# Performance work log

Hardware: AMD Instinct MI355X
Metric: run time of the kernel (lower is better)

Reference implementation:

```python
import jax, jax.numpy as jnp
import numpy as np

B, S, H, NH, PF, L = 2, 2048, 1024, 16, 4096, 6
HD = H // NH
EPS = 1e-5


def setup_inputs() -> dict:
    key = jax.random.key(0)
    ks = jax.random.split(key, 12)
    s = lambda k, shp, fan: jax.random.normal(k, shp, jnp.float32) * (1.0 / np.sqrt(fan))
    return {
        "input_tensor": jax.random.normal(ks[0], (B, S, H), jnp.float32),
        "pos_emb": s(ks[1], (S, H), H),
        "Wq": s(ks[2], (L, H, H), H), "bq": jnp.zeros((L, H), jnp.float32),
        "Wk": s(ks[3], (L, H, H), H), "bk": jnp.zeros((L, H), jnp.float32),
        "Wv": s(ks[4], (L, H, H), H), "bv": jnp.zeros((L, H), jnp.float32),
        "Wo": s(ks[5], (L, H, H), H), "bo": jnp.zeros((L, H), jnp.float32),
        "ln_g": jnp.ones((L, H), jnp.float32), "ln_b": jnp.zeros((L, H), jnp.float32),
        "W1": s(ks[6], (L, H, PF), H), "b1": jnp.zeros((L, PF), jnp.float32),
        "W2": s(ks[7], (L, PF, H), PF), "b2": jnp.zeros((L, H), jnp.float32),
    }


def _layernorm(x, g, b):
    mu = jnp.mean(x, axis=-1, keepdims=True)
    var = jnp.mean(jnp.square(x - mu), axis=-1, keepdims=True)
    return (x - mu) * jax.lax.rsqrt(var + EPS) * g + b


def _encoder(input_tensor, pos_emb, params):
    # pos embed: same positions for every batch row
    src = input_tensor * jnp.sqrt(jnp.float32(H)) + pos_emb[None, :, :]

    def layer(src, p):
        Wq, bq, Wk, bk, Wv, bv, Wo, bo, g, b, W1, b1, W2, b2 = p
        q = (src @ Wq + bq).reshape(B, S, NH, HD)
        k = (src @ Wk + bk).reshape(B, S, NH, HD)
        v = (src @ Wv + bv).reshape(B, S, NH, HD)
        # scores [B, NH, S, S]
        energy = jnp.einsum("bqhd,bkhd->bhqk", q, k) / jnp.sqrt(jnp.float32(HD))
        attn = jax.nn.softmax(energy, axis=-1)
        ctx = jnp.einsum("bhqk,bkhd->bqhd", attn, v).reshape(B, S, H)
        attn_out = ctx @ Wo + bo
        src = _layernorm(src + attn_out, g, b)
        ffn = jax.nn.relu(src @ W1 + b1) @ W2 + b2
        src = _layernorm(src + ffn, g, b)  # same LayerNorm reused, as in source
        return src, None

    src, _ = jax.lax.scan(layer, src, params)
    return src


def reference(input_tensor, pos_emb, Wq, bq, Wk, bk, Wv, bv, Wo, bo, ln_g, ln_b, W1, b1, W2, b2):
    params = (Wq, bq, Wk, bk, Wv, bv, Wo, bo, ln_g, ln_b, W1, b1, W2, b2)
    return _encoder(input_tensor, pos_emb, params)
```

## Files before the change

kernel.cpp:

```cpp
#include <hip/hip_runtime.h>
#include <cstdint>

constexpr int Bc = 2, Sc = 2048, Hc = 1024, NHc = 16, HDc = 64, PFc = 4096, Lc = 6;
constexpr float EPSc = 1e-5f;
constexpr float QSC = 0.18033688011112042f;

using f32x4  = __attribute__((ext_vector_type(4))) float;
using bf16x8 = __attribute__((ext_vector_type(8))) __bf16;
using bf16x4 = __attribute__((ext_vector_type(4))) __bf16;
using u32x4  = __attribute__((ext_vector_type(4))) unsigned;

#if __has_builtin(__builtin_amdgcn_exp2f)
#define EXP2(x) __builtin_amdgcn_exp2f(x)
#else
#define EXP2(x) exp2f(x)
#endif

__device__ __forceinline__ f32x4 mfma16(bf16x8 a, bf16x8 b, f32x4 c) {
    return __builtin_amdgcn_mfma_f32_16x16x32_bf16(a, b, c, 0, 0, 0);
}

__device__ __forceinline__ void gload_lds16(const void* g, void* l) {
    __builtin_amdgcn_global_load_lds(
        (__attribute__((address_space(1))) void*)(uintptr_t)g,
        (__attribute__((address_space(3))) void*)(uint32_t)(uintptr_t)l,
        16, 0, 0);
}

template<int N> __device__ __forceinline__ void wait_vmcnt() {
    if constexpr (N == 0)      asm volatile("s_waitcnt vmcnt(0)" ::: "memory");
    else if constexpr (N == 6) asm volatile("s_waitcnt vmcnt(6)" ::: "memory");
    else if constexpr (N == 8) asm volatile("s_waitcnt vmcnt(8)" ::: "memory");
}
__device__ __forceinline__ void wait_lgkm0() {
    asm volatile("s_waitcnt lgkmcnt(0)" ::: "memory");
    __builtin_amdgcn_sched_barrier(0);
}

struct HL { __bf16 h, l; };
__device__ __forceinline__ HL split2(float v) {
    HL r;
    r.h = (__bf16)v;
    r.l = (__bf16)(v - (float)r.h);
    return r;
}

__device__ __forceinline__ unsigned bfbits(__bf16 x) {
    return (unsigned)__builtin_bit_cast(unsigned short, x);
}
__device__ __forceinline__ unsigned packbf(float a, float b) {
    return bfbits((__bf16)a) | (bfbits((__bf16)b) << 16);
}

__device__ __forceinline__ int xcd_swz(int bid, int nwg) {
    return (bid & 7) * (nwg >> 3) + (bid >> 3);
}

__global__ __launch_bounds__(256) void wconv_kernel(
    const float* __restrict__ in, __bf16* __restrict__ out, int K, int N)
{
    __shared__ float tile[64][65];
    const int t = threadIdx.x;
    const size_t lstride = (size_t)K * N;
    const float* ip = in + (size_t)blockIdx.z * lstride;
    __bf16* op = out + (size_t)blockIdx.z * lstride;
    const int n0 = blockIdx.x * 64, k0 = blockIdx.y * 64;
    #pragma unroll
    for (int c = 0; c < 4; ++c) {
        int idx = c * 256 + t;
        int row = idx >> 4;
        int c4  = idx & 15;
        float4 v = *(const float4*)(ip + (size_t)(k0 + row) * N + n0 + c4 * 4);
        tile[row][c4 * 4 + 0] = v.x; tile[row][c4 * 4 + 1] = v.y;
        tile[row][c4 * 4 + 2] = v.z; tile[row][c4 * 4 + 3] = v.w;
    }
    __syncthreads();
    #pragma unroll
    for (int c = 0; c < 4; ++c) {
        int idx = c * 256 + t;
        int n  = idx >> 4;
        int k4 = idx & 15;
        bf16x4 hh = { (__bf16)tile[k4 * 4 + 0][n], (__bf16)tile[k4 * 4 + 1][n],
                      (__bf16)tile[k4 * 4 + 2][n], (__bf16)tile[k4 * 4 + 3][n] };
        *(bf16x4*)(op + (size_t)(n0 + n) * K + k0 + k4 * 4) = hh;
    }
}

__global__ __launch_bounds__(256) void wconv2_kernel(
    const float* __restrict__ in, __bf16* __restrict__ outh,
    __bf16* __restrict__ outl, int K, int N)
{
    __shared__ float tile[64][65];
    const int t = threadIdx.x;
    const int n0 = blockIdx.x * 64, k0 = blockIdx.y * 64;
    #pragma unroll
    for (int c = 0; c < 4; ++c) {
        int idx = c * 256 + t;
        int row = idx >> 4;
        int c4  = idx & 15;
        float4 v = *(const float4*)(in + (size_t)(k0 + row) * N + n0 + c4 * 4);
        tile[row][c4 * 4 + 0] = v.x; tile[row][c4 * 4 + 1] = v.y;
        tile[row][c4 * 4 + 2] = v.z; tile[row][c4 * 4 + 3] = v.w;
    }
    __syncthreads();
    #pragma unroll
    for (int c = 0; c < 4; ++c) {
        int idx = c * 256 + t;
        int n  = idx >> 4;
        int k4 = idx & 15;
        HL e0 = split2(tile[k4 * 4 + 0][n]);
        HL e1 = split2(tile[k4 * 4 + 1][n]);
        HL e2 = split2(tile[k4 * 4 + 2][n]);
        HL e3 = split2(tile[k4 * 4 + 3][n]);
        bf16x4 hh = { e0.h, e1.h, e2.h, e3.h };
        bf16x4 ll = { e0.l, e1.l, e2.l, e3.l };
        *(bf16x4*)(outh + (size_t)(n0 + n) * K + k0 + k4 * 4) = hh;
        *(bf16x4*)(outl + (size_t)(n0 + n) * K + k0 + k4 * 4) = ll;
    }
}

__global__ __launch_bounds__(256) void embed_kernel(
    const float* __restrict__ in, const float* __restrict__ pos,
    float* __restrict__ sf, __bf16* __restrict__ sh, __bf16* __restrict__ sl)
{
    const int n4 = (Bc * Sc * Hc) / 4;
    const int pmask = (Sc * Hc / 4) - 1;
    for (int i = blockIdx.x * 256 + threadIdx.x; i < n4; i += gridDim.x * 256) {
        float4 a = ((const float4*)in)[i];
        float4 p = ((const float4*)pos)[i & pmask];
        float4 r;
        r.x = a.x * 32.f + p.x; r.y = a.y * 32.f + p.y;
        r.z = a.z * 32.f + p.z; r.w = a.w * 32.f + p.w;
        ((float4*)sf)[i] = r;
        HL e0 = split2(r.x), e1 = split2(r.y), e2 = split2(r.z), e3 = split2(r.w);
        bf16x4 hh = { e0.h, e1.h, e2.h, e3.h };
        bf16x4 ll = { e0.l, e1.l, e2.l, e3.l };
        ((bf16x4*)sh)[i] = hh;
        ((bf16x4*)sl)[i] = ll;
    }
}

template<int BM, int OUTMODE, bool RELU>
__global__ __launch_bounds__(256) void gemm_bt_kernel(
    const __bf16* __restrict__ A, const __bf16* __restrict__ Wt,
    const float* __restrict__ bias, void* __restrict__ out,
    int M, int N, int K)
{
    constexpr int MI = BM / 32;
    constexpr int LPT = BM / 32 + 4;
    __shared__ alignas(16) __bf16 Alds[2][BM * 64];
    __shared__ alignas(16) __bf16 Blds[2][128 * 64];

    const int tid = threadIdx.x, lane = tid & 63, wave = tid >> 6;
    const int lr = lane & 15, lg = lane >> 4;
    const int nbx = gridDim.x;
    const int swz = xcd_swz(blockIdx.y * nbx + blockIdx.x, nbx * gridDim.y);
    const int m0 = (swz / nbx) * BM, n0 = (swz % nbx) * 128;
    const int wm = (wave >> 1) * (BM / 2), wn = (wave & 1) * 64;

    f32x4 acc[MI][4] = {};

    auto stage = [&](int k0, int buf) {
        #pragma unroll
        for (int c = 0; c < BM / 32; ++c) {
            int li = c * 256 + tid;
            int row = li >> 3;
            int lcb = ((li & 7) << 4) ^ ((row & 7) << 4);
            gload_lds16(A + (size_t)(m0 + row) * K + k0 + (lcb >> 1),
                        (char*)Alds[buf] + (size_t)(c * 256 + wave * 64) * 16);
        }
        #pragma unroll
        for (int c = 0; c < 4; ++c) {
            int li = c * 256 + tid;
            int row = li >> 3;
            int lcb = ((li & 7) << 4) ^ ((row & 7) << 4);
            gload_lds16(Wt + (size_t)(n0 + row) * K + k0 + (lcb >> 1),
                        (char*)Blds[buf] + (size_t)(c * 256 + wave * 64) * 16);
        }
    };

    stage(0, 0);
    if (K > 64) stage(64, 1);

    for (int k0 = 0; k0 < K; k0 += 64) {
        const int cur = (k0 >> 6) & 1;
        if (k0 + 64 < K) wait_vmcnt<LPT>();
        else             wait_vmcnt<0>();
        __builtin_amdgcn_s_barrier();

        bf16x8 af[2][MI], bfr[2][4];
        #pragma unroll
        for (int ks = 0; ks < 2; ++ks) {
            #pragma unroll
            for (int i = 0; i < MI; ++i) {
                int ra = wm + i * 16 + lr;
                int pa = (ks * 64 + lg * 16) ^ ((ra & 7) << 4);
                af[ks][i] = *(const bf16x8*)((const char*)Alds[cur] + ra * 128 + pa);
            }
            #pragma unroll
            for (int i = 0; i < 4; ++i) {
                int rb = wn + i * 16 + lr;
                int pb = (ks * 64 + lg * 16) ^ ((rb & 7) << 4);
                bfr[ks][i] = *(const bf16x8*)((const char*)Blds[cur] + rb * 128 + pb);
            }
        }
        wait_lgkm0();
        __builtin_amdgcn_s_barrier();
        if (k0 + 128 < K) stage(k0 + 128, cur);

        __builtin_amdgcn_s_setprio(1);
        #pragma unroll
        for (int ks = 0; ks < 2; ++ks)
            #pragma unroll
            for (int mi = 0; mi < MI; ++mi)
                #pragma unroll
                for (int ni = 0; ni < 4; ++ni)
                    acc[mi][ni] = mfma16(af[ks][mi], bfr[ks][ni], acc[mi][ni]);
        __builtin_amdgcn_s_setprio(0);
    }

    #pragma unroll
    for (int ni = 0; ni < 4; ++ni) {
        int col = n0 + wn + ni * 16 + lr;
        float bv = bias[col];
        #pragma unroll
        for (int mi = 0; mi < MI; ++mi) {
            int rowb = m0 + wm + mi * 16 + lg * 4;
            #pragma unroll
            for (int r = 0; r < 4; ++r) {
                float v = acc[mi][ni][r] + bv;
                if (RELU) v = fmaxf(v, 0.f);
                size_t idx = (size_t)(rowb + r) * N + col;
                if constexpr (OUTMODE == 0) ((float*)out)[idx] = v;
                else                        ((__bf16*)out)[idx] = (__bf16)v;
            }
        }
    }
}

template<int OUTMODE, bool RELU>
__global__ __launch_bounds__(512) void gemm_bt256_kernel(
    const __bf16* __restrict__ A, const __bf16* __restrict__ Wt,
    const float* __restrict__ bias, void* __restrict__ out,
    int M, int N, int K)
{
    constexpr int LPT = 6;
    __shared__ alignas(16) __bf16 Alds[2][256 * 64];
    __shared__ alignas(16) __bf16 Blds[2][128 * 64];

    const int tid = threadIdx.x, lane = tid & 63, wave = tid >> 6;
    const int lr = lane & 15, lg = lane >> 4;
    const int nbx = gridDim.x;
    const int swz = xcd_swz(blockIdx.y * nbx + blockIdx.x, nbx * gridDim.y);
    const int m0 = (swz / nbx) * 256, n0 = (swz % nbx) * 128;
    const int wm = (wave >> 1) * 64, wn = (wave & 1) * 64;

    f32x4 acc[4][4] = {};

    auto stage = [&](int k0, int buf) {
        #pragma unroll
        for (int c = 0; c < 4; ++c) {
            int li = c * 512 + tid;
            int row = li >> 3;
            int lcb = ((li & 7) << 4) ^ ((row & 7) << 4);
            gload_lds16(A + (size_t)(m0 + row) * K + k0 + (lcb >> 1),
                        (char*)Alds[buf] + (size_t)(c * 512 + wave * 64) * 16);
        }
        #pragma unroll
        for (int c = 0; c < 2; ++c) {
            int li = c * 512 + tid;
            int row = li >> 3;
            int lcb = ((li & 7) << 4) ^ ((row & 7) << 4);
            gload_lds16(Wt + (size_t)(n0 + row) * K + k0 + (lcb >> 1),
                        (char*)Blds[buf] + (size_t)(c * 512 + wave * 64) * 16);
        }
    };

    stage(0, 0);
    if (K > 64) stage(64, 1);

    for (int k0 = 0; k0 < K; k0 += 64) {
        const int cur = (k0 >> 6) & 1;
        if (k0 + 64 < K) wait_vmcnt<LPT>();
        else             wait_vmcnt<0>();
        __builtin_amdgcn_s_barrier();

        bf16x8 af[2][4], bfr[2][4];
        #pragma unroll
        for (int ks = 0; ks < 2; ++ks) {
            #pragma unroll
            for (int i = 0; i < 4; ++i) {
                int ra = wm + i * 16 + lr;
                int pa = (ks * 64 + lg * 16) ^ ((ra & 7) << 4);
                af[ks][i] = *(const bf16x8*)((const char*)Alds[cur] + ra * 128 + pa);
                int rb = wn + i * 16 + lr;
                int pb = (ks * 64 + lg * 16) ^ ((rb & 7) << 4);
                bfr[ks][i] = *(const bf16x8*)((const char*)Blds[cur] + rb * 128 + pb);
            }
        }
        wait_lgkm0();
        __builtin_amdgcn_s_barrier();
        if (k0 + 128 < K) stage(k0 + 128, cur);

        __builtin_amdgcn_s_setprio(1);
        #pragma unroll
        for (int ks = 0; ks < 2; ++ks)
            #pragma unroll
            for (int mi = 0; mi < 4; ++mi)
                #pragma unroll
                for (int ni = 0; ni < 4; ++ni)
                    acc[mi][ni] = mfma16(af[ks][mi], bfr[ks][ni], acc[mi][ni]);
        __builtin_amdgcn_s_setprio(0);
    }

    #pragma unroll
    for (int ni = 0; ni < 4; ++ni) {
        int col = n0 + wn + ni * 16 + lr;
        float bv = bias[col];
        #pragma unroll
        for (int mi = 0; mi < 4; ++mi) {
            int rowb = m0 + wm + mi * 16 + lg * 4;
            #pragma unroll
            for (int r = 0; r < 4; ++r) {
                float v = acc[mi][ni][r] + bv;
                if (RELU) v = fmaxf(v, 0.f);
                size_t idx = (size_t)(rowb + r) * N + col;
                if constexpr (OUTMODE == 0) ((float*)out)[idx] = v;
                else                        ((__bf16*)out)[idx] = (__bf16)v;
            }
        }
    }
}

struct QKVBT {
    const __bf16 *wq, *wk, *wv;
    const float *bq, *bk, *bv;
    __bf16 *q, *k, *v;
};

__global__ __launch_bounds__(256) void qkv_bt_kernel(
    const __bf16* __restrict__ A, QKVBT a)
{
    constexpr int N = Hc, K = Hc;
    constexpr int LPT = 8;
    __shared__ alignas(16) __bf16 Alds[2][128 * 64];
    __shared__ alignas(16) __bf16 Blds[2][128 * 64];

    const int tid = threadIdx.x, lane = tid & 63, wave = tid >> 6;
    const int lr = lane & 15, lg = lane >> 4;
    const int nbx = gridDim.x;
    const int swz = xcd_swz(blockIdx.y * nbx + blockIdx.x, nbx * gridDim.y);
    const int gx = swz % nbx;
    const int widx = gx >> 3;
    const int n0 = (gx & 7) * 128;
    const int m0 = (swz / nbx) * 128;
    const int wm = (wave >> 1) * 64, wn = (wave & 1) * 64;

    const __bf16* Wt  = (widx == 0) ? a.wq : (widx == 1) ? a.wk : a.wv;
    const float* bias = (widx == 0) ? a.bq : (widx == 1) ? a.bk : a.bv;

    f32x4 acc[4][4] = {};

    auto stage = [&](int k0, int buf) {
        #pragma unroll
        for (int c = 0; c < 4; ++c) {
            int li = c * 256 + tid;
            int row = li >> 3;
            int lcb = ((li & 7) << 4) ^ ((row & 7) << 4);
            gload_lds16(A + (size_t)(m0 + row) * K + k0 + (lcb >> 1),
                        (char*)Alds[buf] + (size_t)(c * 256 + wave * 64) * 16);
            gload_lds16(Wt + (size_t)(n0 + row) * K + k0 + (lcb >> 1),
                        (char*)Blds[buf] + (size_t)(c * 256 + wave * 64) * 16);
        }
    };

    stage(0, 0);
    stage(64, 1);

    for (int k0 = 0; k0 < K; k0 += 64) {
        const int cur = (k0 >> 6) & 1;
        if (k0 + 64 < K) wait_vmcnt<LPT>();
        else             wait_vmcnt<0>();
        __builtin_amdgcn_s_barrier();

        bf16x8 af[2][4], bfr[2][4];
        #pragma unroll
        for (int ks = 0; ks < 2; ++ks) {
            #pragma unroll
            for (int i = 0; i < 4; ++i) {
                int ra = wm + i * 16 + lr;
                int pa = (ks * 64 + lg * 16) ^ ((ra & 7) << 4);
                af[ks][i] = *(const bf16x8*)((const char*)Alds[cur] + ra * 128 + pa);
                int rb = wn + i * 16 + lr;
                int pb = (ks * 64 + lg * 16) ^ ((rb & 7) << 4);
                bfr[ks][i] = *(const bf16x8*)((const char*)Blds[cur] + rb * 128 + pb);
            }
        }
        wait_lgkm0();
        __builtin_amdgcn_s_barrier();
        if (k0 + 128 < K) stage(k0 + 128, cur);

        __builtin_amdgcn_s_setprio(1);
        #pragma unroll
        for (int ks = 0; ks < 2; ++ks)
            #pragma unroll
            for (int mi = 0; mi < 4; ++mi)
                #pragma unroll
                for (int ni = 0; ni < 4; ++ni)
                    acc[mi][ni] = mfma16(af[ks][mi], bfr[ks][ni], acc[mi][ni]);
        __builtin_amdgcn_s_setprio(0);
    }

    __bf16* outp = (widx == 0) ? a.q : (widx == 1) ? a.k : a.v;
    const float osc = (widx == 0) ? QSC : 1.f;
    #pragma unroll
    for (int ni = 0; ni < 4; ++ni) {
        int col = n0 + wn + ni * 16 + lr;
        float bv = bias[col];
        int hh = col >> 6, d = col & 63;
        #pragma unroll
        for (int mi = 0; mi < 4; ++mi) {
            int rowb = m0 + wm + mi * 16 + lg * 4;
            #pragma unroll
            for (int r = 0; r < 4; ++r) {
                int row = rowb + r;
                int bb = row >> 11, s = row & (Sc - 1);
                outp[((size_t)(bb * NHc + hh) * Sc + s) * HDc + d] =
                    (__bf16)((acc[mi][ni][r] + bv) * osc);
            }
        }
    }
}

struct QKV0S {
    const __bf16 *wqh, *wql, *wkh, *wkl, *wv;
    const float *bq, *bk, *bv;
    __bf16 *qh, *ql, *kh, *kl, *vv;
};

__global__ __launch_bounds__(256) void qkv0s_kernel(
    const __bf16* __restrict__ Ahi, const __bf16* __restrict__ Alo, QKV0S a)
{
    constexpr int N = Hc, K = Hc;
    __shared__ alignas(16) __bf16 AldsH[128 * 64];
    __shared__ alignas(16) __bf16 AldsL[128 * 64];
    __shared__ alignas(16) __bf16 BldsH[128 * 64];
    __shared__ alignas(16) __bf16 BldsL[128 * 64];

    const int tid = threadIdx.x, lane = tid & 63, wave = tid >> 6;
    const int lr = lane & 15, lg = lane >> 4;
    const int nbx = gridDim.x;
    const int swz = xcd_swz(blockIdx.y * nbx + blockIdx.x, nbx * gridDim.y);
    const int gx = swz % nbx;
    const int widx = gx >> 3;
    const int n0 = (gx & 7) * 128;
    const int m0 = (swz / nbx) * 128;
    const int wm = (wave >> 1) * 64, wn = (wave & 1) * 64;
    const bool SPLIT = (widx < 2);

    const __bf16* Bh = (widx == 0) ? a.wqh : (widx == 1) ? a.wkh : a.wv;
    const __bf16* Bl = (widx == 0) ? a.wql : a.wkl;
    const float* bias = (widx == 0) ? a.bq : (widx == 1) ? a.bk : a.bv;

    f32x4 acc[4][4] = {};

    for (int k0 = 0; k0 < K; k0 += 64) {
        #pragma unroll
        for (int c = 0; c < 4; ++c) {
            int li = c * 256 + tid;
            int row = li >> 3;
            int lcb = ((li & 7) << 4) ^ ((row & 7) << 4);
            size_t aoff = (size_t)(m0 + row) * K + k0 + (lcb >> 1);
            size_t boff = (size_t)(n0 + row) * K + k0 + (lcb >> 1);
            size_t loff = (size_t)(c * 256 + wave * 64) * 16;
            gload_lds16(Ahi + aoff, (char*)AldsH + loff);
            gload_lds16(Bh + boff, (char*)BldsH + loff);
            if (SPLIT) {
                gload_lds16(Alo + aoff, (char*)AldsL + loff);
                gload_lds16(Bl + boff, (char*)BldsL + loff);
            }
        }
        __syncthreads();

        bf16x8 ah[2][4], al[2][4], bh[2][4], bl[2][4];
        #pragma unroll
        for (int ks = 0; ks < 2; ++ks) {
            #pragma unroll
            for (int i = 0; i < 4; ++i) {
                int ra = wm + i * 16 + lr;
                int pa = (ks * 64 + lg * 16) ^ ((ra & 7) << 4);
                ah[ks][i] = *(const bf16x8*)((const char*)AldsH + ra * 128 + pa);
                int rb = wn + i * 16 + lr;
                int pb = (ks * 64 + lg * 16) ^ ((rb & 7) << 4);
                bh[ks][i] = *(const bf16x8*)((const char*)BldsH + rb * 128 + pb);
                if (SPLIT) {
                    al[ks][i] = *(const bf16x8*)((const char*)AldsL + ra * 128 + pa);
                    bl[ks][i] = *(const bf16x8*)((const char*)BldsL + rb * 128 + pb);
                }
            }
        }
        #pragma unroll
        for (int ks = 0; ks < 2; ++ks)
            #pragma unroll
            for (int mi = 0; mi < 4; ++mi)
                #pragma unroll
                for (int ni = 0; ni < 4; ++ni) {
                    acc[mi][ni] = mfma16(ah[ks][mi], bh[ks][ni], acc[mi][ni]);
                    if (SPLIT) {
                        acc[mi][ni] = mfma16(al[ks][mi], bh[ks][ni], acc[mi][ni]);
                        acc[mi][ni] = mfma16(ah[ks][mi], bl[ks][ni], acc[mi][ni]);
                    }
                }
        __syncthreads();
    }

    __bf16* outh = (widx == 0) ? a.qh : (widx == 1) ? a.kh : a.vv;
    __bf16* outl = (widx == 0) ? a.ql : a.kl;
    const float osc = (widx == 0) ? QSC : 1.f;
    #pragma unroll
    for (int ni = 0; ni < 4; ++ni) {
        int col = n0 + wn + ni * 16 + lr;
        float bv = bias[col];
        int hh = col >> 6, d = col & 63;
        #pragma unroll
        for (int mi = 0; mi < 4; ++mi) {
            int rowb = m0 + wm + mi * 16 + lg * 4;
            #pragma unroll
            for (int r = 0; r < 4; ++r) {
                int row = rowb + r;
                int bb = row >> 11, s = row & (Sc - 1);
                size_t idx = ((size_t)(bb * NHc + hh) * Sc + s) * HDc + d;
                float v = (acc[mi][ni][r] + bv) * osc;
                if (SPLIT) {
                    HL e = split2(v);
                    outh[idx] = e.h;
                    outl[idx] = e.l;
                } else {
                    outh[idx] = (__bf16)v;
                }
            }
        }
    }
}

template<int QKSPLIT, int NH2>
__global__ __launch_bounds__(256) void attn_kernel(
    const __bf16* __restrict__ Qh, const __bf16* __restrict__ Ql,
    const __bf16* __restrict__ Kh, const __bf16* __restrict__ Kl,
    const __bf16* __restrict__ V, __bf16* __restrict__ O)
{
    constexpr int KVB = 64 * NH2;
    __shared__ alignas(16) __bf16 Ksh[2][KVB * 64];
    __shared__ alignas(16) __bf16 Klo[QKSPLIT ? 2 : 1][QKSPLIT ? 64 * 64 : 8];
    __shared__ alignas(16) __bf16 VT[2][NH2][64 * 64];

    const int tid = threadIdx.x;
    const int lane = tid & 63, wave = tid >> 6;
    const int lr = lane & 15, lg = lane >> 4;
    const int flat = blockIdx.x;
    const int hb = flat & 31;
    const int h = hb & 15, b = hb >> 4;
    const int q0 = (flat >> 5) * 128 + wave * 32;

    const size_t headoff = ((size_t)b * NHc + h) * Sc * HDc;
    const __bf16* Qb  = Qh + headoff;
    const __bf16* Kb  = Kh + headoff;
    const __bf16* Klb = QKSPLIT ? (Kl + headoff) : nullptr;
    const __bf16* Vb  = V + headoff;

    const size_t qrowA = (size_t)(q0 + lr) * HDc;
    const size_t qrowB = qrowA + 16 * HDc;
    bf16x8 qfA0 = *(const bf16x8*)(Qb + qrowA + lg * 8);
    bf16x8 qfA1 = *(const bf16x8*)(Qb + qrowA + 32 + lg * 8);
    bf16x8 qfB0 = *(const bf16x8*)(Qb + qrowB + lg * 8);
    bf16x8 qfB1 = *(const bf16x8*)(Qb + qrowB + 32 + lg * 8);
    bf16x8 qlA0, qlA1, qlB0, qlB1;
    if constexpr (QKSPLIT) {
        const __bf16* Qlb = Ql + headoff;
        qlA0 = *(const bf16x8*)(Qlb + qrowA + lg * 8);
        qlA1 = *(const bf16x8*)(Qlb + qrowA + 32 + lg * 8);
        qlB0 = *(const bf16x8*)(Qlb + qrowB + lg * 8);
        qlB1 = *(const bf16x8*)(Qlb + qrowB + 32 + lg * 8);
    }

    const int kp = tid & 31, dblk = tid >> 5;
    const int sp = (kp & 0x11) | ((kp & 0x06) << 1) | ((kp & 0x08) >> 2);

    auto stageK = [&](int kt, int buf) {
        #pragma unroll
        for (int c = 0; c < 2 * NH2; ++c) {
            int li  = c * 256 + tid;
            int row = li >> 3;
            int lcb = ((li & 7) << 4) ^ ((row & 7) << 4);
            size_t goff = (size_t)(kt * KVB + row) * HDc + (lcb >> 1);
            size_t loff = (size_t)(c * 256 + wave * 64) * 16;
            gload_lds16(Kb + goff, (char*)Ksh[buf] + loff);
            if constexpr (QKSPLIT)
                gload_lds16(Klb + goff, (char*)Klo[buf] + loff);
        }
    };
    auto loadV = [&](int kt, int half, bf16x8& va, bf16x8& vb2) {
        const __bf16* vs = Vb + (size_t)(kt * KVB + half * 64 + 2 * kp) * HDc + dblk * 8;
        va  = *(const bf16x8*)vs;
        vb2 = *(const bf16x8*)(vs + HDc);
    };
    auto writeVT = [&](int buf, int half, bf16x8 va, bf16x8 vb2) {
        #pragma unroll
        for (int j = 0; j < 8; ++j) {
            int d = dblk * 8 + j;
            unsigned u = bfbits(va[j]) | (bfbits(vb2[j]) << 16);
            int byte = d * 128 + ((sp * 4) ^ ((d & 7) << 4));
            *(unsigned*)((char*)VT[buf][half] + byte) = u;
        }
    };

    f32x4 oA[4] = {}, oB[4] = {};
    float mA = -1e30f, mB = -1e30f, lsA = 0.f, lsB = 0.f;

    stageK(0, 0);
    {
        bf16x8 va, vb2;
        #pragma unroll
        for (int hf = 0; hf < NH2; ++hf) {
            loadV(0, hf, va, vb2);
            writeVT(0, hf, va, vb2);
        }
    }
    __syncthreads();

    const int NT = Sc / KVB;
    int cur = 0;
    for (int kt = 0; kt < NT; ++kt) {
        const int nb = cur ^ 1;
        const bool pf = (kt + 1 < NT);
        bf16x8 va[NH2], vb2[NH2];
        if (pf) {
            stageK(kt + 1, nb);
            #pragma unroll
            for (int hf = 0; hf < NH2; ++hf) loadV(kt + 1, hf, va[hf], vb2[hf]);
        }

        const char* Kc  = (const char*)Ksh[cur];
        const char* Klc = (const char*)Klo[QKSPLIT ? cur : 0];

        #pragma unroll
        for (int half = 0; half < NH2; ++half) {
            f32x4 sA[4], sB[4];
            __builtin_amdgcn_s_setprio(1);
            #pragma unroll
            for (int kg = 0; kg < 4; ++kg) {
                int ra = half * 64 + kg * 16 + lr;
                int pa0 = (lg * 16) ^ ((ra & 7) << 4);
                int pa1 = (64 + lg * 16) ^ ((ra & 7) << 4);
                bf16x8 kf0 = *(const bf16x8*)(Kc + ra * 128 + pa0);
                bf16x8 kf1 = *(const bf16x8*)(Kc + ra * 128 + pa1);
                f32x4 tA = {}, tB = {};
                tA = mfma16(kf0, qfA0, tA);
                tA = mfma16(kf1, qfA1, tA);
                tB = mfma16(kf0, qfB0, tB);
                tB = mfma16(kf1, qfB1, tB);
                if constexpr (QKSPLIT) {
                    bf16x8 kg0 = *(const bf16x8*)(Klc + ra * 128 + pa0);
                    bf16x8 kg1 = *(const bf16x8*)(Klc + ra * 128 + pa1);
                    tA = mfma16(kg0, qfA0, tA);
                    tA = mfma16(kg1, qfA1, tA);
                    tA = mfma16(kf0, qlA0, tA);
                    tA = mfma16(kf1, qlA1, tA);
                    tB = mfma16(kg0, qfB0, tB);
                    tB = mfma16(kg1, qfB1, tB);
                    tB = mfma16(kf0, qlB0, tB);
                    tB = mfma16(kf1, qlB1, tB);
                }
                sA[kg] = tA;
                sB[kg] = tB;
            }
            __builtin_amdgcn_s_setprio(0);

            float mtA = -1e30f, mtB = -1e30f;
            #pragma unroll
            for (int kg = 0; kg < 4; ++kg)
                #pragma unroll
                for (int r = 0; r < 4; ++r) {
                    mtA = fmaxf(mtA, sA[kg][r]);
                    mtB = fmaxf(mtB, sB[kg][r]);
                }
            mtA = fmaxf(mtA, __shfl_xor(mtA, 16));
            mtA = fmaxf(mtA, __shfl_xor(mtA, 32));
            mtB = fmaxf(mtB, __shfl_xor(mtB, 16));
            mtB = fmaxf(mtB, __shfl_xor(mtB, 32));
            if (!__all(mtA <= mA + 8.f)) {
                float mnew = fmaxf(mA, mtA);
                float fac = EXP2(mA - mnew);
                mA = mnew;
                lsA *= fac;
                #pragma unroll
                for (int r = 0; r < 4; ++r) {
                    float fr = __shfl(fac, (lg << 4) | (lg * 4 + r));
                    #pragma unroll
                    for (int nd = 0; nd < 4; ++nd) oA[nd][r] *= fr;
                }
            }
            if (!__all(mtB <= mB + 8.f)) {
                float mnew = fmaxf(mB, mtB);
                float fac = EXP2(mB - mnew);
                mB = mnew;
                lsB *= fac;
                #pragma unroll
                for (int r = 0; r < 4; ++r) {
                    float fr = __shfl(fac, (lg << 4) | (lg * 4 + r));
                    #pragma unroll
                    for (int nd = 0; nd < 4; ++nd) oB[nd][r] *= fr;
                }
            }
            float psA = 0.f, psB = 0.f;
            #pragma unroll
            for (int kg = 0; kg < 4; ++kg)
                #pragma unroll
                for (int r = 0; r < 4; ++r) {
                    float pA = EXP2(sA[kg][r] - mA);
                    float pB = EXP2(sB[kg][r] - mB);
                    psA += pA;
                    psB += pB;
                    sA[kg][r] = pA;
                    sB[kg][r] = pB;
                }
            psA += __shfl_xor(psA, 16);
            psA += __shfl_xor(psA, 32);
            psB += __shfl_xor(psB, 16);
            psB += __shfl_xor(psB, 32);
            lsA += psA;
            lsB += psB;

            #pragma unroll
            for (int kh2 = 0; kh2 < 2; ++kh2) {
                u32x4 pkA, pkB;
                pkA[0] = packbf(sA[2 * kh2][0],     sA[2 * kh2][1]);
                pkA[1] = packbf(sA[2 * kh2][2],     sA[2 * kh2][3]);
                pkA[2] = packbf(sA[2 * kh2 + 1][0], sA[2 * kh2 + 1][1]);
                pkA[3] = packbf(sA[2 * kh2 + 1][2], sA[2 * kh2 + 1][3]);
                pkB[0] = packbf(sB[2 * kh2][0],     sB[2 * kh2][1]);
                pkB[1] = packbf(sB[2 * kh2][2],     sB[2 * kh2][3]);
                pkB[2] = packbf(sB[2 * kh2 + 1][0], sB[2 * kh2 + 1][1]);
                pkB[3] = packbf(sB[2 * kh2 + 1][2], sB[2 * kh2 + 1][3]);
                bf16x8 pafA = __builtin_bit_cast(bf16x8, pkA);
                bf16x8 pafB = __builtin_bit_cast(bf16x8, pkB);
                __builtin_amdgcn_s_setprio(1);
                #pragma unroll
                for (int nd = 0; nd < 4; ++nd) {
                    int d = nd * 16 + lr;
                    int byte = d * 128 + ((64 * kh2 + 16 * lg) ^ ((d & 7) << 4));
                    bf16x8 vbf = *(const bf16x8*)((const char*)VT[cur][half] + byte);
                    oA[nd] = mfma16(pafA, vbf, oA[nd]);
                    oB[nd] = mfma16(pafB, vbf, oB[nd]);
                }
                __builtin_amdgcn_s_setprio(0);
            }
        }

        if (pf) {
            #pragma unroll
            for (int hf = 0; hf < NH2; ++hf) writeVT(nb, hf, va[hf], vb2[hf]);
        }
        __syncthreads();
        cur = nb;
    }

    #pragma unroll
    for (int r = 0; r < 4; ++r) {
        float lvA = __shfl(lsA, (lg << 4) | (lg * 4 + r));
        float lvB = __shfl(lsB, (lg << 4) | (lg * 4 + r));
        float invA = 1.f / lvA;
        float invB = 1.f / lvB;
        size_t orowA = ((size_t)b * Sc + q0 + lg * 4 + r) * Hc + h * HDc;
        size_t orowB = orowA + (size_t)16 * Hc;
        #pragma unroll
        for (int nd = 0; nd < 4; ++nd) {
            O[orowA + nd * 16 + lr] = (__bf16)(oA[nd][r] * invA);
            O[orowB + nd * 16 + lr] = (__bf16)(oB[nd][r] * invB);
        }
    }
}

__global__ __launch_bounds__(256) void ln_kernel(
    const float* __restrict__ xr, const __bf16* __restrict__ y,
    const float* __restrict__ g, const float* __restrict__ beta,
    float* __restrict__ of, __bf16* __restrict__ oh)
{
    __shared__ float red[2][4];
    const int row = blockIdx.x, t = threadIdx.x;
    const int lane = t & 63, wave = t >> 6;
    const int idx = row * 256 + t;
    float4 a = ((const float4*)xr)[idx];
    bf16x4 cb = ((const bf16x4*)y)[idx];
    float4 v;
    v.x = a.x + (float)cb[0]; v.y = a.y + (float)cb[1];
    v.z = a.z + (float)cb[2]; v.w = a.w + (float)cb[3];
    float s1 = v.x + v.y + v.z + v.w;
    float s2 = v.x * v.x + v.y * v.y + v.z * v.z + v.w * v.w;
    #pragma unroll
    for (int off = 1; off < 64; off <<= 1) {
        s1 += __shfl_xor(s1, off);
        s2 += __shfl_xor(s2, off);
    }
    if (lane == 0) { red[0][wave] = s1; red[1][wave] = s2; }
    __syncthreads();
    s1 = red[0][0] + red[0][1] + red[0][2] + red[0][3];
    s2 = red[1][0] + red[1][1] + red[1][2] + red[1][3];
    const float mu   = s1 * (1.f / Hc);
    const float var  = s2 * (1.f / Hc) - mu * mu;
    const float rstd = rsqrtf(var + EPSc);
    float4 gg = ((const float4*)g)[t];
    float4 bb = ((const float4*)beta)[t];
    float4 r;
    r.x = (v.x - mu) * rstd * gg.x + bb.x;
    r.y = (v.y - mu) * rstd * gg.y + bb.y;
    r.z = (v.z - mu) * rstd * gg.z + bb.z;
    r.w = (v.w - mu) * rstd * gg.w + bb.w;
    ((float4*)of)[idx] = r;
    bf16x4 hh = { (__bf16)r.x, (__bf16)r.y, (__bf16)r.z, (__bf16)r.w };
    ((bf16x4*)oh)[idx] = hh;
}

extern "C" void kernel_launch(void* const* d_in, const int* in_sizes, int n_in,
                              void* d_out, int out_size, void* d_ws, size_t ws_size,
                              hipStream_t stream)
{
    const float* inp = (const float*)d_in[0];
    const float* pos = (const float*)d_in[1];
    const float* Wq  = (const float*)d_in[2];
    const float* bq  = (const float*)d_in[3];
    const float* Wk  = (const float*)d_in[4];
    const float* bk  = (const float*)d_in[5];
    const float* Wv  = (const float*)d_in[6];
    const float* bv  = (const float*)d_in[7];
    const float* Wo  = (const float*)d_in[8];
    const float* bo  = (const float*)d_in[9];
    const float* lng = (const float*)d_in[10];
    const float* lnb = (const float*)d_in[11];
    const float* W1  = (const float*)d_in[12];
    const float* b1  = (const float*)d_in[13];
    const float* W2  = (const float*)d_in[14];
    const float* b2  = (const float*)d_in[15];

    char* ws = (char*)d_ws;
    const size_t MB = 1u << 20;
    float*  src_f = (float*)(ws);
    __bf16* src_h = (__bf16*)(ws + 16 * MB);
    __bf16* src_l = (__bf16*)(ws + 24 * MB);
    __bf16* qh    = (__bf16*)(ws + 32 * MB);
    __bf16* kh    = (__bf16*)(ws + 40 * MB);
    __bf16* vv    = (__bf16*)(ws + 48 * MB);
    __bf16* ctx   = (__bf16*)(ws + 56 * MB);
    __bf16* ql    = (__bf16*)(ws + 64 * MB);
    __bf16* kl    = (__bf16*)(ws + 72 * MB);
    __bf16* tmpb  = (__bf16*)(ws + 80 * MB);
    __bf16* wq0h  = (__bf16*)(ws + 80 * MB);
    __bf16* wq0l  = (__bf16*)(ws + 82 * MB);
    __bf16* wk0h  = (__bf16*)(ws + 84 * MB);
    __bf16* wk0l  = (__bf16*)(ws + 86 * MB);
    __bf16* h1    = (__bf16*)(ws + 32 * MB);
    __bf16* wqT   = (__bf16*)(ws + 96 * MB);
    __bf16* wkT   = (__bf16*)(ws + 108 * MB);
    __bf16* wvT   = (__bf16*)(ws + 120 * MB);
    __bf16* woT   = (__bf16*)(ws + 132 * MB);
    __bf16* w1T   = (__bf16*)(ws + 144 * MB);
    __bf16* w2T   = (__bf16*)(ws + 192 * MB);

    const int M = Bc * Sc;

    wconv_kernel<<<dim3(16, 16, 5), 256, 0, stream>>>(Wq + (size_t)Hc * Hc,
                                                      wqT + (size_t)Hc * Hc, Hc, Hc);
    wconv_kernel<<<dim3(16, 16, 5), 256, 0, stream>>>(Wk + (size_t)Hc * Hc,
                                                      wkT + (size_t)Hc * Hc, Hc, Hc);
    wconv_kernel<<<dim3(16, 16, 6), 256, 0, stream>>>(Wv, wvT, Hc, Hc);
    wconv_kernel<<<dim3(16, 16, 6), 256, 0, stream>>>(Wo, woT, Hc, Hc);
    wconv_kernel<<<dim3(64, 16, 6), 256, 0, stream>>>(W1, w1T, Hc, PFc);
    wconv_kernel<<<dim3(16, 64, 6), 256, 0, stream>>>(W2, w2T, PFc, Hc);
    wconv2_kernel<<<dim3(16, 16), 256, 0, stream>>>(Wq, wq0h, wq0l, Hc, Hc);
    wconv2_kernel<<<dim3(16, 16), 256, 0, stream>>>(Wk, wk0h, wk0l, Hc, Hc);

    embed_kernel<<<2048, 256, 0, stream>>>(inp, pos, src_f, src_h, src_l);

    for (int l = 0; l < Lc; ++l) {
        const size_t wHH = (size_t)l * Hc * Hc;
        const size_t wH  = (size_t)l * Hc;
        if (l == 0) {
            QKV0S qa = { wq0h, wq0l, wk0h, wk0l, wvT, bq, bk, bv,
                         qh, ql, kh, kl, vv };
            qkv0s_kernel<<<dim3(24, 32), 256, 0, stream>>>(src_h, src_l, qa);
            attn_kernel<1, 1><<<512, 256, 0, stream>>>(qh, ql, kh, kl, vv, ctx);
        } else {
            QKVBT qa = { wqT + wHH, wkT + wHH, wvT + wHH, bq + wH, bk + wH, bv + wH,
                         qh, kh, vv };
            qkv_bt_kernel<<<dim3(24, 32), 256, 0, stream>>>(src_h, qa);
            attn_kernel<0, 2><<<512, 256, 0, stream>>>(qh, nullptr, kh, nullptr, vv, ctx);
        }
        gemm_bt_kernel<64, 1, false><<<dim3(8, 64), 256, 0, stream>>>(
            ctx, woT + wHH, bo + wH, tmpb, M, Hc, Hc);
        ln_kernel<<<M, 256, 0, stream>>>(src_f, tmpb, lng + wH, lnb + wH, src_f, src_h);
        gemm_bt256_kernel<1, true><<<dim3(32, 16), 512, 0, stream>>>(
            src_h, w1T + (size_t)l * Hc * PFc, b1 + (size_t)l * PFc, h1, M, PFc, Hc);
        gemm_bt_kernel<64, 1, false><<<dim3(8, 64), 256, 0, stream>>>(
            h1, w2T + (size_t)l * PFc * Hc, b2 + wH, tmpb, M, Hc, PFc);
        float* dst = (l == Lc - 1) ? (float*)d_out : src_f;
        ln_kernel<<<M, 256, 0, stream>>>(src_f, tmpb, lng + wH, lnb + wH, dst, src_h);
    }
}
```

Baseline: 1.516 ms.

## Split-K the FFN down-projection and fuse partial sums into LayerNorm

Replaces the FFN second GEMM with a split-K=2 kernel using 64x128 tiles, writing two bf16 partial outputs, and adds an ln3 kernel that sums both partials with the residual before normalizing. The W1 GEMM switches from the 256-row 512-thread tile to the generic 128-row tile kernel. The aim is more blocks in flight for the long-K GEMM on the many CUs. In exchange it adds partial-output traffic and rounds each partial to bf16.

```diff
diff --git a/kernel.cpp b/kernel.cpp
--- a/kernel.cpp
+++ b/kernel.cpp
@@ -238,61 +238,67 @@
     }
 }
 
-template<int OUTMODE, bool RELU>
-__global__ __launch_bounds__(512) void gemm_bt256_kernel(
+__global__ __launch_bounds__(256) void gemm_btsk_kernel(
     const __bf16* __restrict__ A, const __bf16* __restrict__ Wt,
-    const float* __restrict__ bias, void* __restrict__ out,
-    int M, int N, int K)
-{
+    const float* __restrict__ bias, __bf16* __restrict__ out,
+    int M, int N, int K, int KL)
+{
+    constexpr int MI = 2;
     constexpr int LPT = 6;
-    __shared__ alignas(16) __bf16 Alds[2][256 * 64];
+    __shared__ alignas(16) __bf16 Alds[2][64 * 64];
     __shared__ alignas(16) __bf16 Blds[2][128 * 64];
 
     const int tid = threadIdx.x, lane = tid & 63, wave = tid >> 6;
     const int lr = lane & 15, lg = lane >> 4;
     const int nbx = gridDim.x;
     const int swz = xcd_swz(blockIdx.y * nbx + blockIdx.x, nbx * gridDim.y);
-    const int m0 = (swz / nbx) * 256, n0 = (swz % nbx) * 128;
-    const int wm = (wave >> 1) * 64, wn = (wave & 1) * 64;
-
-    f32x4 acc[4][4] = {};
+    const int m0 = (swz / nbx) * 64, n0 = (swz % nbx) * 128;
+    const int wm = (wave >> 1) * 32, wn = (wave & 1) * 64;
+    const int koff = blockIdx.z * KL;
+    const int kend = koff + KL;
+    __bf16* outz = out + (size_t)blockIdx.z * M * N;
+
+    f32x4 acc[MI][4] = {};
 
     auto stage = [&](int k0, int buf) {
         #pragma unroll
-        for (int c = 0; c < 4; ++c) {
-            int li = c * 512 + tid;
+        for (int c = 0; c < 2; ++c) {
+            int li = c * 256 + tid;
             int row = li >> 3;
             int lcb = ((li & 7) << 4) ^ ((row & 7) << 4);
             gload_lds16(A + (size_t)(m0 + row) * K + k0 + (lcb >> 1),
-                        (char*)Alds[buf] + (size_t)(c * 512 + wave * 64) * 16);
-        }
-        #pragma unroll
-        for (int c = 0; c < 2; ++c) {
-            int li = c * 512 + tid;
+                        (char*)Alds[buf] + (size_t)(c * 256 + wave * 64) * 16);
+        }
+        #pragma unroll
+        for (int c = 0; c < 4; ++c) {
+            int li = c * 256 + tid;
             int row = li >> 3;
             int lcb = ((li & 7) << 4) ^ ((row & 7) << 4);
             gload_lds16(Wt + (size_t)(n0 + row) * K + k0 + (lcb >> 1),
-                        (char*)Blds[buf] + (size_t)(c * 512 + wave * 64) * 16);
+                        (char*)Blds[buf] + (size_t)(c * 256 + wave * 64) * 16);
         }
     };
 
-    stage(0, 0);
-    if (K > 64) stage(64, 1);
-
-    for (int k0 = 0; k0 < K; k0 += 64) {
-        const int cur = (k0 >> 6) & 1;
-        if (k0 + 64 < K) wait_vmcnt<LPT>();
-        else             wait_vmcnt<0>();
+    stage(koff, 0);
+    stage(koff + 64, 1);
+
+    for (int k0 = koff; k0 < kend; k0 += 64) {
+        const int cur = ((k0 - koff) >> 6) & 1;
+        if (k0 + 64 < kend) wait_vmcnt<LPT>();
+        else                wait_vmcnt<0>();
         __builtin_amdgcn_s_barrier();
 
-        bf16x8 af[2][4], bfr[2][4];
+        bf16x8 af[2][MI], bfr[2][4];
         #pragma unroll
         for (int ks = 0; ks < 2; ++ks) {
             #pragma unroll
-            for (int i = 0; i < 4; ++i) {
+            for (int i = 0; i < MI; ++i) {
                 int ra = wm + i * 16 + lr;
                 int pa = (ks * 64 + lg * 16) ^ ((ra & 7) << 4);
                 af[ks][i] = *(const bf16x8*)((const char*)Alds[cur] + ra * 128 + pa);
+            }
+            #pragma unroll
+            for (int i = 0; i < 4; ++i) {
                 int rb = wn + i * 16 + lr;
                 int pb = (ks * 64 + lg * 16) ^ ((rb & 7) << 4);
                 bfr[ks][i] = *(const bf16x8*)((const char*)Blds[cur] + rb * 128 + pb);
@@ -300,13 +306,13 @@
         }
         wait_lgkm0();
         __builtin_amdgcn_s_barrier();
-        if (k0 + 128 < K) stage(k0 + 128, cur);
+        if (k0 + 128 < kend) stage(k0 + 128, cur);
 
         __builtin_amdgcn_s_setprio(1);
         #pragma unroll
         for (int ks = 0; ks < 2; ++ks)
             #pragma unroll
-            for (int mi = 0; mi < 4; ++mi)
+            for (int mi = 0; mi < MI; ++mi)
                 #pragma unroll
                 for (int ni = 0; ni < 4; ++ni)
                     acc[mi][ni] = mfma16(af[ks][mi], bfr[ks][ni], acc[mi][ni]);
@@ -316,18 +322,13 @@
     #pragma unroll
     for (int ni = 0; ni < 4; ++ni) {
         int col = n0 + wn + ni * 16 + lr;
-        float bv = bias[col];
-        #pragma unroll
-        for (int mi = 0; mi < 4; ++mi) {
+        float bv = (blockIdx.z == 0) ? bias[col] : 0.f;
+        #pragma unroll
+        for (int mi = 0; mi < MI; ++mi) {
             int rowb = m0 + wm + mi * 16 + lg * 4;
             #pragma unroll
-            for (int r = 0; r < 4; ++r) {
-                float v = acc[mi][ni][r] + bv;
-                if (RELU) v = fmaxf(v, 0.f);
-                size_t idx = (size_t)(rowb + r) * N + col;
-                if constexpr (OUTMODE == 0) ((float*)out)[idx] = v;
-                else                        ((__bf16*)out)[idx] = (__bf16)v;
-            }
+            for (int r = 0; r < 4; ++r)
+                outz[(size_t)(rowb + r) * N + col] = (__bf16)(acc[mi][ni][r] + bv);
         }
     }
 }
@@ -821,6 +822,50 @@
     ((bf16x4*)oh)[idx] = hh;
 }
 
+__global__ __launch_bounds__(256) void ln3_kernel(
+    const float* __restrict__ xr, const __bf16* __restrict__ y1,
+    const __bf16* __restrict__ y2,
+    const float* __restrict__ g, const float* __restrict__ beta,
+    float* __restrict__ of, __bf16* __restrict__ oh)
+{
+    __shared__ float red[2][4];
+    const int row = blockIdx.x, t = threadIdx.x;
+    const int lane = t & 63, wave = t >> 6;
+    const int idx = row * 256 + t;
+    float4 a = ((const float4*)xr)[idx];
+    bf16x4 c1 = ((const bf16x4*)y1)[idx];
+    bf16x4 c2 = ((const bf16x4*)y2)[idx];
+    float4 v;
+    v.x = a.x + (float)c1[0] + (float)c2[0];
+    v.y = a.y + (float)c1[1] + (float)c2[1];
+    v.z = a.z + (float)c1[2] + (float)c2[2];
+    v.w = a.w + (float)c1[3] + (float)c2[3];
+    float s1 = v.x + v.y + v.z + v.w;
+    float s2 = v.x * v.x + v.y * v.y + v.z * v.z + v.w * v.w;
+    #pragma unroll
+    for (int off = 1; off < 64; off <<= 1) {
+        s1 += __shfl_xor(s1, off);
+        s2 += __shfl_xor(s2, off);
+    }
+    if (lane == 0) { red[0][wave] = s1; red[1][wave] = s2; }
+    __syncthreads();
+    s1 = red[0][0] + red[0][1] + red[0][2] + red[0][3];
+    s2 = red[1][0] + red[1][1] + red[1][2] + red[1][3];
+    const float mu   = s1 * (1.f / Hc);
+    const float var  = s2 * (1.f / Hc) - mu * mu;
+    const float rstd = rsqrtf(var + EPSc);
+    float4 gg = ((const float4*)g)[t];
+    float4 bb = ((const float4*)beta)[t];
+    float4 r;
+    r.x = (v.x - mu) * rstd * gg.x + bb.x;
+    r.y = (v.y - mu) * rstd * gg.y + bb.y;
+    r.z = (v.z - mu) * rstd * gg.z + bb.z;
+    r.w = (v.w - mu) * rstd * gg.w + bb.w;
+    ((float4*)of)[idx] = r;
+    bf16x4 hh = { (__bf16)r.x, (__bf16)r.y, (__bf16)r.z, (__bf16)r.w };
+    ((bf16x4*)oh)[idx] = hh;
+}
+
 extern "C" void kernel_launch(void* const* d_in, const int* in_sizes, int n_in,
                               void* d_out, int out_size, void* d_ws, size_t ws_size,
                               hipStream_t stream)
@@ -858,6 +903,7 @@
     __bf16* wq0l  = (__bf16*)(ws + 82 * MB);
     __bf16* wk0h  = (__bf16*)(ws + 84 * MB);
     __bf16* wk0l  = (__bf16*)(ws + 86 * MB);
+    __bf16* tmpb2 = (__bf16*)(ws + 88 * MB);
     __bf16* h1    = (__bf16*)(ws + 32 * MB);
     __bf16* wqT   = (__bf16*)(ws + 96 * MB);
     __bf16* wkT   = (__bf16*)(ws + 108 * MB);
@@ -898,11 +944,11 @@
         gemm_bt_kernel<64, 1, false><<<dim3(8, 64), 256, 0, stream>>>(
             ctx, woT + wHH, bo + wH, tmpb, M, Hc, Hc);
         ln_kernel<<<M, 256, 0, stream>>>(src_f, tmpb, lng + wH, lnb + wH, src_f, src_h);
-        gemm_bt256_kernel<1, true><<<dim3(32, 16), 512, 0, stream>>>(
+        gemm_bt_kernel<128, 1, true><<<dim3(32, 32), 256, 0, stream>>>(
             src_h, w1T + (size_t)l * Hc * PFc, b1 + (size_t)l * PFc, h1, M, PFc, Hc);
-        gemm_bt_kernel<64, 1, false><<<dim3(8, 64), 256, 0, stream>>>(
-            h1, w2T + (size_t)l * PFc * Hc, b2 + wH, tmpb, M, Hc, PFc);
+        gemm_btsk_kernel<<<dim3(8, 64, 2), 256, 0, stream>>>(
+            h1, w2T + (size_t)l * PFc * Hc, b2 + wH, tmpb, M, Hc, PFc, PFc / 2);
         float* dst = (l == Lc - 1) ? (float*)d_out : src_f;
-        ln_kernel<<<M, 256, 0, stream>>>(src_f, tmpb, lng + wH, lnb + wH, dst, src_h);
-    }
-}
+        ln3_kernel<<<M, 256, 0, stream>>>(src_f, tmpb, tmpb2, lng + wH, lnb + wH, dst, src_h);
+    }
+}
```

Result: no change. 1.528 ms (+0.8%).

## Replace FFN1 GEMM with 256x256 tile, 8-wave ping-pong schedule

Applied to the files above, without the earlier changes.

The FFN up-projection GEMM moves from a 256x128 tile to a 256x256 tile on 8 waves arranged 2x4. Each wave computes a 128x64 sub-tile in four MFMA quarter-phases, and LDS fragment loads and global-to-LDS staging of A and B are interleaved between those phases. The aim is higher arithmetic intensity per loaded byte and better overlap of loads with MFMA work. In exchange it uses more accumulator registers, 128KB of LDS, many extra barriers, and only 256 blocks for the grid, which may reduce occupancy.

```diff
diff --git a/kernel.cpp b/kernel.cpp
--- a/kernel.cpp
+++ b/kernel.cpp
@@ -29,6 +29,7 @@
 
 template<int N> __device__ __forceinline__ void wait_vmcnt() {
     if constexpr (N == 0)      asm volatile("s_waitcnt vmcnt(0)" ::: "memory");
+    else if constexpr (N == 4) asm volatile("s_waitcnt vmcnt(4)" ::: "memory");
     else if constexpr (N == 6) asm volatile("s_waitcnt vmcnt(6)" ::: "memory");
     else if constexpr (N == 8) asm volatile("s_waitcnt vmcnt(8)" ::: "memory");
 }
@@ -239,87 +240,149 @@
 }
 
 template<int OUTMODE, bool RELU>
-__global__ __launch_bounds__(512) void gemm_bt256_kernel(
+__global__ __launch_bounds__(512, 2) void gemm8p_kernel(
     const __bf16* __restrict__ A, const __bf16* __restrict__ Wt,
     const float* __restrict__ bias, void* __restrict__ out,
     int M, int N, int K)
 {
-    constexpr int LPT = 6;
-    __shared__ alignas(16) __bf16 Alds[2][256 * 64];
-    __shared__ alignas(16) __bf16 Blds[2][128 * 64];
+    __shared__ alignas(16) __bf16 AL[2][2][128 * 64];
+    __shared__ alignas(16) __bf16 BL[2][2][128 * 64];
 
     const int tid = threadIdx.x, lane = tid & 63, wave = tid >> 6;
     const int lr = lane & 15, lg = lane >> 4;
+    const int wr = wave >> 2, wc = wave & 3;
     const int nbx = gridDim.x;
     const int swz = xcd_swz(blockIdx.y * nbx + blockIdx.x, nbx * gridDim.y);
-    const int m0 = (swz / nbx) * 256, n0 = (swz % nbx) * 128;
-    const int wm = (wave >> 1) * 64, wn = (wave & 1) * 64;
-
-    f32x4 acc[4][4] = {};
-
-    auto stage = [&](int k0, int buf) {
-        #pragma unroll
-        for (int c = 0; c < 4; ++c) {
-            int li = c * 512 + tid;
-            int row = li >> 3;
-            int lcb = ((li & 7) << 4) ^ ((row & 7) << 4);
-            gload_lds16(A + (size_t)(m0 + row) * K + k0 + (lcb >> 1),
-                        (char*)Alds[buf] + (size_t)(c * 512 + wave * 64) * 16);
-        }
+    const int m0 = (swz / nbx) * 256, n0 = (swz % nbx) * 256;
+    const int NT = K >> 6;
+    const int brow = (wc & 1) * 64;
+
+    f32x4 acc[8][4] = {};
+
+    auto stageA = [&](int t, int half) {
         #pragma unroll
         for (int c = 0; c < 2; ++c) {
             int li = c * 512 + tid;
             int row = li >> 3;
             int lcb = ((li & 7) << 4) ^ ((row & 7) << 4);
-            gload_lds16(Wt + (size_t)(n0 + row) * K + k0 + (lcb >> 1),
-                        (char*)Blds[buf] + (size_t)(c * 512 + wave * 64) * 16);
+            gload_lds16(A + (size_t)(m0 + half * 128 + row) * K + t * 64 + (lcb >> 1),
+                        (char*)AL[t & 1][half] + (size_t)(c * 512 + wave * 64) * 16);
         }
     };
-
-    stage(0, 0);
-    if (K > 64) stage(64, 1);
-
-    for (int k0 = 0; k0 < K; k0 += 64) {
-        const int cur = (k0 >> 6) & 1;
-        if (k0 + 64 < K) wait_vmcnt<LPT>();
-        else             wait_vmcnt<0>();
-        __builtin_amdgcn_s_barrier();
-
-        bf16x8 af[2][4], bfr[2][4];
+    auto stageB = [&](int t, int half) {
+        #pragma unroll
+        for (int c = 0; c < 2; ++c) {
+            int li = c * 512 + tid;
+            int row = li >> 3;
+            int lcb = ((li & 7) << 4) ^ ((row & 7) << 4);
+            gload_lds16(Wt + (size_t)(n0 + half * 128 + row) * K + t * 64 + (lcb >> 1),
+                        (char*)BL[t & 1][half] + (size_t)(c * 512 + wave * 64) * 16);
+        }
+    };
+
+    stageA(0, 0); stageA(0, 1); stageB(0, 0); stageB(0, 1);
+    if (NT > 1) { stageA(1, 0); stageA(1, 1); }
+
+    bf16x8 af[2][4], b0[2][2], b1[2][2];
+
+    for (int t = 0; t < NT; ++t) {
+        const char* Ah = (const char*)AL[t & 1][wr];
+        const char* Bh = (const char*)BL[t & 1][wc >> 1];
+
+        if (t == NT - 1) wait_vmcnt<0>(); else wait_vmcnt<4>();
+        __builtin_amdgcn_s_barrier();
         #pragma unroll
         for (int ks = 0; ks < 2; ++ks) {
             #pragma unroll
             for (int i = 0; i < 4; ++i) {
-                int ra = wm + i * 16 + lr;
-                int pa = (ks * 64 + lg * 16) ^ ((ra & 7) << 4);
-                af[ks][i] = *(const bf16x8*)((const char*)Alds[cur] + ra * 128 + pa);
-                int rb = wn + i * 16 + lr;
-                int pb = (ks * 64 + lg * 16) ^ ((rb & 7) << 4);
-                bfr[ks][i] = *(const bf16x8*)((const char*)Blds[cur] + rb * 128 + pb);
-            }
-        }
+                int row = i * 16 + lr;
+                af[ks][i] = *(const bf16x8*)(Ah + row * 128 +
+                            ((ks * 64 + lg * 16) ^ ((row & 7) << 4)));
+            }
+            #pragma unroll
+            for (int j = 0; j < 2; ++j) {
+                int row = brow + j * 16 + lr;
+                b0[ks][j] = *(const bf16x8*)(Bh + row * 128 +
+                            ((ks * 64 + lg * 16) ^ ((row & 7) << 4)));
+            }
+        }
+        if (t + 1 < NT) { stageB(t + 1, 0); stageB(t + 1, 1); }
+        __builtin_amdgcn_s_barrier();
         wait_lgkm0();
-        __builtin_amdgcn_s_barrier();
-        if (k0 + 128 < K) stage(k0 + 128, cur);
-
         __builtin_amdgcn_s_setprio(1);
         #pragma unroll
         for (int ks = 0; ks < 2; ++ks)
             #pragma unroll
             for (int mi = 0; mi < 4; ++mi)
                 #pragma unroll
-                for (int ni = 0; ni < 4; ++ni)
-                    acc[mi][ni] = mfma16(af[ks][mi], bfr[ks][ni], acc[mi][ni]);
+                for (int j = 0; j < 2; ++j)
+                    acc[mi][j] = mfma16(af[ks][mi], b0[ks][j], acc[mi][j]);
         __builtin_amdgcn_s_setprio(0);
+        __builtin_amdgcn_s_barrier();
+
+        #pragma unroll
+        for (int ks = 0; ks < 2; ++ks)
+            #pragma unroll
+            for (int j = 0; j < 2; ++j) {
+                int row = brow + (2 + j) * 16 + lr;
+                b1[ks][j] = *(const bf16x8*)(Bh + row * 128 +
+                            ((ks * 64 + lg * 16) ^ ((row & 7) << 4)));
+            }
+        __builtin_amdgcn_s_barrier();
+        wait_lgkm0();
+        __builtin_amdgcn_s_setprio(1);
+        #pragma unroll
+        for (int ks = 0; ks < 2; ++ks)
+            #pragma unroll
+            for (int mi = 0; mi < 4; ++mi)
+                #pragma unroll
+                for (int j = 0; j < 2; ++j)
+                    acc[mi][2 + j] = mfma16(af[ks][mi], b1[ks][j], acc[mi][2 + j]);
+        __builtin_amdgcn_s_setprio(0);
+        __builtin_amdgcn_s_barrier();
+
+        #pragma unroll
+        for (int ks = 0; ks < 2; ++ks)
+            #pragma unroll
+            for (int i = 0; i < 4; ++i) {
+                int row = (4 + i) * 16 + lr;
+                af[ks][i] = *(const bf16x8*)(Ah + row * 128 +
+                            ((ks * 64 + lg * 16) ^ ((row & 7) << 4)));
+            }
+        __builtin_amdgcn_s_barrier();
+        wait_lgkm0();
+        __builtin_amdgcn_s_setprio(1);
+        #pragma unroll
+        for (int ks = 0; ks < 2; ++ks)
+            #pragma unroll
+            for (int mi = 0; mi < 4; ++mi)
+                #pragma unroll
+                for (int j = 0; j < 2; ++j)
+                    acc[4 + mi][2 + j] = mfma16(af[ks][mi], b1[ks][j], acc[4 + mi][2 + j]);
+        __builtin_amdgcn_s_setprio(0);
+        __builtin_amdgcn_s_barrier();
+
+        if (t + 2 < NT) { stageA(t + 2, 0); stageA(t + 2, 1); }
+        __builtin_amdgcn_s_barrier();
+        __builtin_amdgcn_s_setprio(1);
+        #pragma unroll
+        for (int ks = 0; ks < 2; ++ks)
+            #pragma unroll
+            for (int mi = 0; mi < 4; ++mi)
+                #pragma unroll
+                for (int j = 0; j < 2; ++j)
+                    acc[4 + mi][j] = mfma16(af[ks][mi], b0[ks][j], acc[4 + mi][j]);
+        __builtin_amdgcn_s_setprio(0);
+        __builtin_amdgcn_s_barrier();
     }
 
     #pragma unroll
     for (int ni = 0; ni < 4; ++ni) {
-        int col = n0 + wn + ni * 16 + lr;
+        int col = n0 + wc * 64 + ni * 16 + lr;
         float bv = bias[col];
         #pragma unroll
-        for (int mi = 0; mi < 4; ++mi) {
-            int rowb = m0 + wm + mi * 16 + lg * 4;
+        for (int mi = 0; mi < 8; ++mi) {
+            int rowb = m0 + wr * 128 + mi * 16 + lg * 4;
             #pragma unroll
             for (int r = 0; r < 4; ++r) {
                 float v = acc[mi][ni][r] + bv;
@@ -898,7 +961,7 @@
         gemm_bt_kernel<64, 1, false><<<dim3(8, 64), 256, 0, stream>>>(
             ctx, woT + wHH, bo + wH, tmpb, M, Hc, Hc);
         ln_kernel<<<M, 256, 0, stream>>>(src_f, tmpb, lng + wH, lnb + wH, src_f, src_h);
-        gemm_bt256_kernel<1, true><<<dim3(32, 16), 512, 0, stream>>>(
+        gemm8p_kernel<1, true><<<dim3(16, 16), 512, 0, stream>>>(
             src_h, w1T + (size_t)l * Hc * PFc, b1 + (size_t)l * PFc, h1, M, PFc, Hc);
         gemm_bt_kernel<64, 1, false><<<dim3(8, 64), 256, 0, stream>>>(
             h1, w2T + (size_t)l * PFc * Hc, b2 + wH, tmpb, M, Hc, PFc);
```

Result: faster. 1.472 ms (-2.9%).
